# Kernel optimization log

Measured on AMD Instinct MI355X. Metric: run time of the kernel, lower is better.

The kernel has to match this reference:

```python
import jax, jax.numpy as jnp
from jax import lax
import numpy as np

H = 64
NS = 20000
NR = 2000
T = 24
ALPHA = 0.5


def _p(key, *shape):
    return jax.random.normal(key, shape, dtype=jnp.float32) * 0.05


def setup_inputs() -> dict:
    key = jax.random.key(0)
    ks = jax.random.split(key, 40)
    inp = {
        "x_store": jax.random.normal(ks[0], (NS, T), dtype=jnp.float32),
        "x_region": jax.random.normal(ks[1], (NR, T), dtype=jnp.float32),
        "edge_ss": jax.random.randint(ks[2], (2, 640000), 0, NS),
        "edge_rs_src": jax.random.randint(ks[3], (160000,), 0, NR),
        "edge_rs_dst": jax.random.randint(ks[4], (160000,), 0, NS),
        "edge_sr_src": jax.random.randint(ks[5], (160000,), 0, NS),
        "edge_sr_dst": jax.random.randint(ks[6], (160000,), 0, NR),
        # LSTM pretransform params (torch gate order i,f,g,o)
        "Wih_s": _p(ks[7], 4 * H, 1), "Whh_s": _p(ks[8], 4 * H, H),
        "bih_s": _p(ks[9], 4 * H), "bhh_s": _p(ks[10], 4 * H),
        "Wih_r": _p(ks[11], 4 * H, 1), "Whh_r": _p(ks[12], 4 * H, H),
        "bih_r": _p(ks[13], 4 * H), "bhh_r": _p(ks[14], 4 * H),
        # DirSageConv (store-store)
        "W_s2d": _p(ks[15], H, H), "b_s2d": _p(ks[16], H),
        "W_d2s": _p(ks[17], H, H), "b_d2s": _p(ks[18], H),
        "W_self": _p(ks[19], H, H), "b_self": _p(ks[20], H),
        # SAGEConv region->store (lin_l w/ bias, lin_r no bias)
        "Wl_rs": _p(ks[21], H, H), "bl_rs": _p(ks[22], H), "Wr_rs": _p(ks[23], H, H),
        # SAGEConv store->region
        "Wl_sr": _p(ks[24], H, H), "bl_sr": _p(ks[25], H), "Wr_sr": _p(ks[26], H, H),
        # final linear
        "Wf": _p(ks[27], H, H), "bf": _p(ks[28], H),
    }
    return inp


def lstm_last(x, Wih, Whh, bih, bhh):
    # x: [N, T] scalar sequences (input_size=1). Returns last hidden state [N, H].
    N = x.shape[0]
    w_in = Wih[:, 0]  # [4H]
    b = bih + bhh

    def step(carry, xt):
        h, c = carry
        gates = xt[:, None] * w_in[None, :] + h @ Whh.T + b  # [N, 4H]
        i, f, g, o = jnp.split(gates, 4, axis=1)
        c = jax.nn.sigmoid(f) * c + jax.nn.sigmoid(i) * jnp.tanh(g)
        h = jax.nn.sigmoid(o) * jnp.tanh(c)
        return (h, c), None

    z = jnp.zeros((N, Whh.shape[1]), x.dtype)
    (h, _), _ = lax.scan(step, (z, z), x.T)
    return h


def mean_aggr(feats, dst_idx, num_dst):
    # mean of gathered edge messages per destination node (0 for isolated nodes)
    s = jax.ops.segment_sum(feats, dst_idx, num_segments=num_dst)
    cnt = jax.ops.segment_sum(jnp.ones(dst_idx.shape, feats.dtype), dst_idx, num_segments=num_dst)
    return s / jnp.maximum(cnt, 1.0)[:, None]


def reference(x_store, x_region, edge_ss, edge_rs_src, edge_rs_dst,
              edge_sr_src, edge_sr_dst,
              Wih_s, Whh_s, bih_s, bhh_s, Wih_r, Whh_r, bih_r, bhh_r,
              W_s2d, b_s2d, W_d2s, b_d2s, W_self, b_self,
              Wl_rs, bl_rs, Wr_rs, Wl_sr, bl_sr, Wr_sr, Wf, bf):
    # per-node-type LSTM pretransform -> [N, H]
    hs = lstm_last(x_store, Wih_s, Whh_s, bih_s, bhh_s)
    hr = lstm_last(x_region, Wih_r, Whh_r, bih_r, bhh_r)

    # DirSageConv on (store, link, store)
    src, dst = edge_ss[0], edge_ss[1]
    a_fwd = mean_aggr(hs[src], dst, NS) @ W_s2d.T + b_s2d   # src -> dst
    a_rev = mean_aggr(hs[dst], src, NS) @ W_d2s.T + b_d2s   # dst -> src
    dir_out = hs @ W_self.T + b_self + (1.0 - ALPHA) * a_fwd + ALPHA * a_rev

    # SAGEConv (region, influences, store)
    rs_out = mean_aggr(hr[edge_rs_src], edge_rs_dst, NS) @ Wl_rs.T + bl_rs + hs @ Wr_rs.T

    # SAGEConv (store, rev_influences, region)
    sr_out = mean_aggr(hs[edge_sr_src], edge_sr_dst, NR) @ Wl_sr.T + bl_sr + hr @ Wr_sr.T

    # HeteroConv aggr='mean' over edge types per dst node type
    store_h = (dir_out + rs_out) * 0.5
    region_h = sr_out

    # residual + relu
    store_h = jax.nn.relu(store_h + hs)
    region_h = jax.nn.relu(region_h + hr)  # computed as in torch, unused by output

    return store_h @ Wf.T + bf
```

## Files before the change

kernel.cpp:

```cpp
#include <hip/hip_runtime.h>
#include <hip/hip_bf16.h>

#define TT 24
#define NSTORE 20000
#define NREGION 2000
#define NE_SS 640000
#define NE_RS 160000
#define BN 32
#define CAPF 80
#define CAPS 32
#define POISON ((int)0xAAAAAAAAu)

typedef __attribute__((ext_vector_type(8))) short bf16x8;
typedef __attribute__((ext_vector_type(4))) float f32x4;
typedef __attribute__((ext_vector_type(4))) int int4v;

__device__ __forceinline__ float rcpf(float x) { return __builtin_amdgcn_rcpf(x); }
__device__ __forceinline__ float sigm(float x) { return rcpf(1.0f + __expf(-x)); }
__device__ __forceinline__ float tanh_(float x) { return fmaf(-2.0f, rcpf(1.0f + __expf(2.0f * x)), 1.0f); }

__device__ __forceinline__ short f2bs(float x) {
    __hip_bfloat16 h = __float2bfloat16(x);
    return *reinterpret_cast<short*>(&h);
}
__device__ __forceinline__ bf16x8 pack8(float4 a, float4 b) {
    bf16x8 r;
    r[0] = f2bs(a.x); r[1] = f2bs(a.y); r[2] = f2bs(a.z); r[3] = f2bs(a.w);
    r[4] = f2bs(b.x); r[5] = f2bs(b.y); r[6] = f2bs(b.z); r[7] = f2bs(b.w);
    return r;
}
__device__ __forceinline__ unsigned packbf2(float lo, float hi) {
    return ((unsigned)(unsigned short)f2bs(hi) << 16) | (unsigned)(unsigned short)f2bs(lo);
}
__device__ __forceinline__ float bf_lo(unsigned u) { return __uint_as_float(u << 16); }
__device__ __forceinline__ float bf_hi(unsigned u) { return __uint_as_float(u & 0xffff0000u); }

__device__ __forceinline__ f32x4 mfma16(bf16x8 a, bf16x8 b, f32x4 c) {
    return __builtin_amdgcn_mfma_f32_16x16x32_bf16(a, b, c, 0, 0, 0);
}

__global__ __launch_bounds__(256)
void lstm_fill(const float* __restrict__ xs, const float* __restrict__ WihS,
               const float* __restrict__ WhhS, const float* __restrict__ bihS,
               const float* __restrict__ bhhS,
               const float* __restrict__ xr, const float* __restrict__ WihR,
               const float* __restrict__ WhhR, const float* __restrict__ bihR,
               const float* __restrict__ bhhR,
               unsigned* __restrict__ hsOut, unsigned* __restrict__ hrOut,
               const int* __restrict__ ss_src, const int* __restrict__ ss_dst,
               const int* __restrict__ rs_src, const int* __restrict__ rs_dst,
               int* __restrict__ curF, int* __restrict__ curR, int* __restrict__ curS,
               int* __restrict__ eidF, int* __restrict__ eidR, int* __restrict__ eidS,
               int nBlocksStore, int nBlocksLstm)
{
    const int tid = threadIdx.x;

    if ((int)blockIdx.x >= nBlocksLstm) {
        const int u = ((int)blockIdx.x - nBlocksLstm) * 256 + tid;
        if (u < NE_SS / 4) {
            const int4v s4 = __builtin_nontemporal_load(&((const int4v*)ss_src)[u]);
            const int4v d4 = __builtin_nontemporal_load(&((const int4v*)ss_dst)[u]);
            int pf0 = atomicAdd(&curF[d4[0]], 1) - POISON;
            int pf1 = atomicAdd(&curF[d4[1]], 1) - POISON;
            int pf2 = atomicAdd(&curF[d4[2]], 1) - POISON;
            int pf3 = atomicAdd(&curF[d4[3]], 1) - POISON;
            int pr0 = atomicAdd(&curR[s4[0]], 1) - POISON;
            int pr1 = atomicAdd(&curR[s4[1]], 1) - POISON;
            int pr2 = atomicAdd(&curR[s4[2]], 1) - POISON;
            int pr3 = atomicAdd(&curR[s4[3]], 1) - POISON;
            if (pf0 < CAPF) eidF[d4[0] * CAPF + pf0] = s4[0];
            if (pf1 < CAPF) eidF[d4[1] * CAPF + pf1] = s4[1];
            if (pf2 < CAPF) eidF[d4[2] * CAPF + pf2] = s4[2];
            if (pf3 < CAPF) eidF[d4[3] * CAPF + pf3] = s4[3];
            if (pr0 < CAPF) eidR[s4[0] * CAPF + pr0] = d4[0];
            if (pr1 < CAPF) eidR[s4[1] * CAPF + pr1] = d4[1];
            if (pr2 < CAPF) eidR[s4[2] * CAPF + pr2] = d4[2];
            if (pr3 < CAPF) eidR[s4[3] * CAPF + pr3] = d4[3];
        } else if (u < (NE_SS + NE_RS) / 4) {
            const int v = u - NE_SS / 4;
            const int4v s4 = __builtin_nontemporal_load(&((const int4v*)rs_src)[v]);
            const int4v d4 = __builtin_nontemporal_load(&((const int4v*)rs_dst)[v]);
            int p0 = atomicAdd(&curS[d4[0]], 1) - POISON;
            int p1 = atomicAdd(&curS[d4[1]], 1) - POISON;
            int p2 = atomicAdd(&curS[d4[2]], 1) - POISON;
            int p3 = atomicAdd(&curS[d4[3]], 1) - POISON;
            if (p0 < CAPS) eidS[d4[0] * CAPS + p0] = s4[0];
            if (p1 < CAPS) eidS[d4[1] * CAPS + p1] = s4[1];
            if (p2 < CAPS) eidS[d4[2] * CAPS + p2] = s4[2];
            if (p3 < CAPS) eidS[d4[3] * CAPS + p3] = s4[3];
        }
        return;
    }

    __shared__ unsigned hbU[2][32][36];
    __shared__ float xbuf[BN][25];

    const float *x, *Wih, *Whh, *bih, *bhh;
    unsigned* hout; int N, node0;
    if ((int)blockIdx.x < nBlocksStore) {
        x = xs; Wih = WihS; Whh = WhhS; bih = bihS; bhh = bhhS;
        hout = hsOut; N = NSTORE; node0 = blockIdx.x * BN;
    } else {
        x = xr; Wih = WihR; Whh = WhhR; bih = bihR; bhh = bhhR;
        hout = hrOut; N = NREGION; node0 = ((int)blockIdx.x - nBlocksStore) * BN;
    }

    const int w = tid >> 6, lane = tid & 63;
    const int l15 = lane & 15, q = lane >> 4;

    for (int i = tid; i < BN * TT; i += 256) {
        int n = i / TT, t = i - n * TT;
        int gn = node0 + n;
        xbuf[n][t] = (gn < N) ? x[gn * TT + t] : 0.0f;
    }

    bf16x8 Bf[4][2];
    #pragma unroll
    for (int g = 0; g < 4; ++g)
        #pragma unroll
        for (int kt = 0; kt < 2; ++kt) {
            const float* wrow = Whh + (g * 64 + (w << 4) + l15) * 64 + q * 8 + kt * 32;
            float4 v0 = *(const float4*)wrow;
            float4 v1 = *(const float4*)(wrow + 4);
            Bf[g][kt] = pack8(v0, v1);
        }

    float win[4], bsum[4];
    #pragma unroll
    for (int g = 0; g < 4; ++g) {
        int gi = g * 64 + (w << 4) + l15;
        win[g]  = Wih[gi];
        bsum[g] = bih[gi] + bhh[gi];
    }

    __syncthreads();

    float cc[2][4], hv[2][4];
    #pragma unroll
    for (int m = 0; m < 2; ++m)
        #pragma unroll
        for (int r = 0; r < 4; ++r) cc[m][r] = 0.0f;

    for (int t = 0; t < TT; ++t) {
        const int cur = t & 1, prev = cur ^ 1;

        bf16x8 Af[2][2];
        if (t > 0) {
            #pragma unroll
            for (int m = 0; m < 2; ++m)
                #pragma unroll
                for (int kt = 0; kt < 2; ++kt)
                    Af[m][kt] = *(const bf16x8*)&hbU[prev][l15 + 16 * m][(q << 2) + (kt << 4)];
        }

        f32x4 acc[4][2];
        float xv[2][4];
        #pragma unroll
        for (int m = 0; m < 2; ++m)
            #pragma unroll
            for (int r = 0; r < 4; ++r) xv[m][r] = xbuf[16 * m + q * 4 + r][t];
        #pragma unroll
        for (int g = 0; g < 4; ++g)
            #pragma unroll
            for (int m = 0; m < 2; ++m)
                #pragma unroll
                for (int r = 0; r < 4; ++r)
                    acc[g][m][r] = fmaf(xv[m][r], win[g], bsum[g]);

        if (t > 0) {
            #pragma unroll
            for (int g = 0; g < 4; ++g)
                #pragma unroll
                for (int m = 0; m < 2; ++m) {
                    acc[g][m] = mfma16(Af[m][0], Bf[g][0], acc[g][m]);
                    acc[g][m] = mfma16(Af[m][1], Bf[g][1], acc[g][m]);
                }
        }

        #pragma unroll
        for (int m = 0; m < 2; ++m)
            #pragma unroll
            for (int r = 0; r < 4; ++r) {
                float ig = sigm(acc[0][m][r]);
                float fg = sigm(acc[1][m][r]);
                float gg = tanh_(acc[2][m][r]);
                float og = sigm(acc[3][m][r]);
                float cn = fmaf(fg, cc[m][r], ig * gg);
                cc[m][r] = cn;
                hv[m][r] = og * tanh_(cn);
            }

        #pragma unroll
        for (int m = 0; m < 2; ++m)
            #pragma unroll
            for (int r = 0; r < 4; ++r) {
                float other = __shfl_xor(hv[m][r], 1);
                if ((l15 & 1) == 0)
                    hbU[cur][16 * m + 4 * q + r][(w << 3) + (l15 >> 1)] = packbf2(hv[m][r], other);
            }
        __syncthreads();
    }

    for (int i = tid; i < 32 * 32; i += 256) {
        int n = i >> 5, kp = i & 31;
        int gn = node0 + n;
        if (gn < N) hout[gn * 32 + kp] = hbU[1][n][kp];
    }
}

__global__ __launch_bounds__(256)
void gather_means(const unsigned* __restrict__ hsU, const unsigned* __restrict__ hrU,
                  const int* __restrict__ curF, const int* __restrict__ curR,
                  const int* __restrict__ curS,
                  const int* __restrict__ eidF, const int* __restrict__ eidR,
                  const int* __restrict__ eidS,
                  unsigned* __restrict__ xcatU)
{
    const int id = blockIdx.x * 4 + (threadIdx.x >> 6);
    const int lane = threadIdx.x & 63;
    const int sec = id / NSTORE;
    const int n   = id - sec * NSTORE;
    const int o8 = lane >> 3, l7 = lane & 7;

    unsigned* row = xcatU + (size_t)n * 128;

    if (sec == 0 && lane < 32) row[lane] = hsU[n * 32 + lane];

    const unsigned* feat = (sec == 2) ? hrU : hsU;
    const int* seg; int cnt, cap;
    if (sec == 0)      { seg = eidF + n * CAPF; cnt = curF[n] - POISON; cap = CAPF; }
    else if (sec == 1) { seg = eidR + n * CAPF; cnt = curR[n] - POISON; cap = CAPF; }
    else               { seg = eidS + n * CAPS; cnt = curS[n] - POISON; cap = CAPS; }
    int e = cnt < cap ? cnt : cap;

    float a[8];
    #pragma unroll
    for (int k = 0; k < 8; ++k) a[k] = 0.0f;

    for (int i = 0; i < e; i += 16) {
        int i0 = i + o8;
        if (i0 < e) {
            uint4 u = *(const uint4*)&feat[seg[i0] * 32 + 4 * l7];
            a[0] += bf_lo(u.x); a[1] += bf_hi(u.x);
            a[2] += bf_lo(u.y); a[3] += bf_hi(u.y);
            a[4] += bf_lo(u.z); a[5] += bf_hi(u.z);
            a[6] += bf_lo(u.w); a[7] += bf_hi(u.w);
        }
        int i1 = i + 8 + o8;
        if (i1 < e) {
            uint4 u = *(const uint4*)&feat[seg[i1] * 32 + 4 * l7];
            a[0] += bf_lo(u.x); a[1] += bf_hi(u.x);
            a[2] += bf_lo(u.y); a[3] += bf_hi(u.y);
            a[4] += bf_lo(u.z); a[5] += bf_hi(u.z);
            a[6] += bf_lo(u.w); a[7] += bf_hi(u.w);
        }
    }
    #pragma unroll
    for (int k = 0; k < 8; ++k) {
        a[k] += __shfl_xor(a[k], 8);
        a[k] += __shfl_xor(a[k], 16);
        a[k] += __shfl_xor(a[k], 32);
    }
    float c = rcpf(fmaxf((float)cnt, 1.0f));
    if (lane < 8) {
        uint4 o;
        o.x = packbf2(a[0] * c, a[1] * c);
        o.y = packbf2(a[2] * c, a[3] * c);
        o.z = packbf2(a[4] * c, a[5] * c);
        o.w = packbf2(a[6] * c, a[7] * c);
        *(uint4*)&row[(sec + 1) * 32 + 4 * l7] = o;
    }
}

__global__ __launch_bounds__(256, 3)
void combine_mm(const unsigned* __restrict__ xcatU,
                const float* __restrict__ Ws2d, const float* __restrict__ bs2d,
                const float* __restrict__ Wd2s, const float* __restrict__ bd2s,
                const float* __restrict__ Wself, const float* __restrict__ bself,
                const float* __restrict__ Wlrs, const float* __restrict__ blrs,
                const float* __restrict__ Wrrs,
                const float* __restrict__ Wfm, const float* __restrict__ bfv,
                float* __restrict__ out)
{
    __shared__ float Xs[64][36];
    __shared__ float Ps[64][64];
    __shared__ float Us[64][36];
    __shared__ float Wfs[64][68];
    __shared__ float biasc[64];

    const int tid = threadIdx.x;
    const int node0 = blockIdx.x * 32;

    for (int i = tid; i < 4096; i += 256) {
        int jp = i >> 6, j = i & 63;
        Wfs[j][jp] = Wfm[i];
    }
    if (tid < 64)
        biasc[tid] = bself[tid] + 0.5f * bs2d[tid] + 0.5f * bd2s[tid] + blrs[tid];

    const int jg = tid & 15, ng = tid >> 4;
    const int j0 = jg * 4, n0 = ng * 2;

    float acc[2][4];
    #pragma unroll
    for (int dn = 0; dn < 2; ++dn)
        #pragma unroll
        for (int dj = 0; dj < 4; ++dj) acc[dn][dj] = 0.0f;

    const int sj = tid >> 2, skb = tid & 3;

    for (int ci = 0; ci < 4; ++ci) {
        const int c = (ci + 1) & 3;
        __syncthreads();

        {
            int n = tid >> 3;
            int gn = node0 + n; if (gn > NSTORE - 1) gn = NSTORE - 1;
            const unsigned* src = xcatU + (size_t)gn * 128 + c * 32 + (tid & 7) * 4;
            uint4 u = *(const uint4*)src;
            unsigned uu[4] = {u.x, u.y, u.z, u.w};
            int k0 = (tid & 7) * 8;
            #pragma unroll
            for (int e = 0; e < 4; ++e) {
                Xs[k0 + 2 * e][n]     = bf_lo(uu[e]);
                Xs[k0 + 2 * e + 1][n] = bf_hi(uu[e]);
            }
        }
        {
            const float* W1; float scale;
            if (c == 0)      { W1 = Wself; scale = 1.0f; }
            else if (c == 1) { W1 = Ws2d;  scale = 0.5f; }
            else if (c == 2) { W1 = Wd2s;  scale = 0.5f; }
            else             { W1 = Wlrs;  scale = 1.0f; }
            #pragma unroll
            for (int qq = 0; qq < 4; ++qq) {
                int k0 = skb * 16 + qq * 4;
                float4 v = *(const float4*)(W1 + sj * 64 + k0);
                if (c == 0) {
                    float4 v2 = *(const float4*)(Wrrs + sj * 64 + k0);
                    v.x += v2.x; v.y += v2.y; v.z += v2.z; v.w += v2.w;
                } else {
                    v.x *= scale; v.y *= scale; v.z *= scale; v.w *= scale;
                }
                Ps[k0][sj] = v.x; Ps[k0 + 1][sj] = v.y;
                Ps[k0 + 2][sj] = v.z; Ps[k0 + 3][sj] = v.w;
            }
        }
        __syncthreads();

        #pragma unroll 4
        for (int k = 0; k < 64; ++k) {
            float4 wv = *(const float4*)&Ps[k][j0];
            float x0 = Xs[k][n0], x1 = Xs[k][n0 + 1];
            float w4[4] = {wv.x, wv.y, wv.z, wv.w};
            #pragma unroll
            for (int dj = 0; dj < 4; ++dj) {
                acc[0][dj] = fmaf(x0, w4[dj], acc[0][dj]);
                acc[1][dj] = fmaf(x1, w4[dj], acc[1][dj]);
            }
        }
    }

    #pragma unroll
    for (int dn = 0; dn < 2; ++dn)
        #pragma unroll
        for (int dj = 0; dj < 4; ++dj) {
            float h = Xs[j0 + dj][n0 + dn];
            float u = fmaxf(fmaf(0.5f, acc[dn][dj] + biasc[j0 + dj], h), 0.0f);
            Us[j0 + dj][n0 + dn] = u;
        }
    __syncthreads();

    float o[2][4];
    #pragma unroll
    for (int dn = 0; dn < 2; ++dn)
        #pragma unroll
        for (int dj = 0; dj < 4; ++dj) o[dn][dj] = 0.0f;

    #pragma unroll 4
    for (int k = 0; k < 64; ++k) {
        float4 wv = *(const float4*)&Wfs[k][j0];
        float u0 = Us[k][n0], u1 = Us[k][n0 + 1];
        float w4[4] = {wv.x, wv.y, wv.z, wv.w};
        #pragma unroll
        for (int dj = 0; dj < 4; ++dj) {
            o[0][dj] = fmaf(u0, w4[dj], o[0][dj]);
            o[1][dj] = fmaf(u1, w4[dj], o[1][dj]);
        }
    }

    float4 bfe = *(const float4*)(bfv + j0);
    #pragma unroll
    for (int dn = 0; dn < 2; ++dn) {
        int gn = node0 + n0 + dn;
        if (gn < NSTORE) {
            float4 v = make_float4(o[dn][0] + bfe.x, o[dn][1] + bfe.y,
                                   o[dn][2] + bfe.z, o[dn][3] + bfe.w);
            *(float4*)&out[gn * 64 + j0] = v;
        }
    }
}

extern "C" void kernel_launch(void* const* d_in, const int* in_sizes, int n_in,
                              void* d_out, int out_size, void* d_ws, size_t ws_size,
                              hipStream_t stream)
{
    const float* xs     = (const float*)d_in[0];
    const float* xr     = (const float*)d_in[1];
    const int*   e_ss   = (const int*)d_in[2];
    const int*   rs_src = (const int*)d_in[3];
    const int*   rs_dst = (const int*)d_in[4];
    const float* WihS = (const float*)d_in[7];
    const float* WhhS = (const float*)d_in[8];
    const float* bihS = (const float*)d_in[9];
    const float* bhhS = (const float*)d_in[10];
    const float* WihR = (const float*)d_in[11];
    const float* WhhR = (const float*)d_in[12];
    const float* bihR = (const float*)d_in[13];
    const float* bhhR = (const float*)d_in[14];
    const float* Ws2d = (const float*)d_in[15];
    const float* bs2d = (const float*)d_in[16];
    const float* Wd2s = (const float*)d_in[17];
    const float* bd2s = (const float*)d_in[18];
    const float* Wself = (const float*)d_in[19];
    const float* bself = (const float*)d_in[20];
    const float* Wlrs = (const float*)d_in[21];
    const float* blrs = (const float*)d_in[22];
    const float* Wrrs = (const float*)d_in[23];
    const float* Wfm = (const float*)d_in[27];
    const float* bfv = (const float*)d_in[28];

    const int* ss_src = e_ss;
    const int* ss_dst = e_ss + NE_SS;

    unsigned* hsU   = (unsigned*)d_ws;
    unsigned* hrU   = hsU + 640000;
    unsigned* xcatU = hrU + 64000;
    int*      ib    = (int*)(xcatU + 2560000);
    int* curF = ib;
    int* curR = ib + 20000;
    int* curS = ib + 40000;
    int* eidF = ib + 60000;
    int* eidR = eidF + NSTORE * CAPF;
    int* eidS = eidR + NSTORE * CAPF;

    const int storeBlocks  = (NSTORE + BN - 1) / BN;
    const int regionBlocks = (NREGION + BN - 1) / BN;
    const int lstmBlocks   = storeBlocks + regionBlocks;
    const int fillBlocks   = ((NE_SS + NE_RS) / 4 + 255) / 256;

    lstm_fill<<<lstmBlocks + fillBlocks, 256, 0, stream>>>(
        xs, WihS, WhhS, bihS, bhhS, xr, WihR, WhhR, bihR, bhhR,
        hsU, hrU, ss_src, ss_dst, rs_src, rs_dst,
        curF, curR, curS, eidF, eidR, eidS,
        storeBlocks, lstmBlocks);

    gather_means<<<3 * NSTORE / 4, 256, 0, stream>>>(hsU, hrU,
                                                     curF, curR, curS,
                                                     eidF, eidR, eidS, xcatU);

    combine_mm<<<(NSTORE + 31) / 32, 256, 0, stream>>>(xcatU,
                                                       Ws2d, bs2d, Wd2s, bd2s,
                                                       Wself, bself, Wlrs, blrs, Wrrs,
                                                       Wfm, bfv, (float*)d_out);
}
```

Measured before the change: 261.5 us.

## Fuse neighbor mean gathering into combine matmul kernel via shared memory

Merges the gather_means and combine_mm kernels into one 512-thread kernel. Each block gathers the three neighbor means for its 32 store nodes straight into shared memory in fp32, then runs the weight combine and final linear layer. This removes the xcatU global round trip, the bf16 rounding of the means, and one kernel launch. In exchange there are fewer blocks (625), each block must gather before it can compute with no overlap, and shared memory use per block grows, which may lower occupancy.

```diff
diff --git a/kernel.cpp b/kernel.cpp
--- a/kernel.cpp
+++ b/kernel.cpp
@@ -208,124 +208,106 @@
     }
 }
 
-__global__ __launch_bounds__(256)
-void gather_means(const unsigned* __restrict__ hsU, const unsigned* __restrict__ hrU,
-                  const int* __restrict__ curF, const int* __restrict__ curR,
-                  const int* __restrict__ curS,
-                  const int* __restrict__ eidF, const int* __restrict__ eidR,
-                  const int* __restrict__ eidS,
-                  unsigned* __restrict__ xcatU)
+__global__ __launch_bounds__(512)
+void gather_combine(const unsigned* __restrict__ hsU, const unsigned* __restrict__ hrU,
+                    const int* __restrict__ curF, const int* __restrict__ curR,
+                    const int* __restrict__ curS,
+                    const int* __restrict__ eidF, const int* __restrict__ eidR,
+                    const int* __restrict__ eidS,
+                    const float* __restrict__ Ws2d, const float* __restrict__ bs2d,
+                    const float* __restrict__ Wd2s, const float* __restrict__ bd2s,
+                    const float* __restrict__ Wself, const float* __restrict__ bself,
+                    const float* __restrict__ Wlrs, const float* __restrict__ blrs,
+                    const float* __restrict__ Wrrs,
+                    const float* __restrict__ Wfm, const float* __restrict__ bfv,
+                    float* __restrict__ out)
 {
-    const int id = blockIdx.x * 4 + (threadIdx.x >> 6);
-    const int lane = threadIdx.x & 63;
-    const int sec = id / NSTORE;
-    const int n   = id - sec * NSTORE;
-    const int o8 = lane >> 3, l7 = lane & 7;
-
-    unsigned* row = xcatU + (size_t)n * 128;
-
-    if (sec == 0 && lane < 32) row[lane] = hsU[n * 32 + lane];
-
-    const unsigned* feat = (sec == 2) ? hrU : hsU;
-    const int* seg; int cnt, cap;
-    if (sec == 0)      { seg = eidF + n * CAPF; cnt = curF[n] - POISON; cap = CAPF; }
-    else if (sec == 1) { seg = eidR + n * CAPF; cnt = curR[n] - POISON; cap = CAPF; }
-    else               { seg = eidS + n * CAPS; cnt = curS[n] - POISON; cap = CAPS; }
-    int e = cnt < cap ? cnt : cap;
-
-    float a[8];
-    #pragma unroll
-    for (int k = 0; k < 8; ++k) a[k] = 0.0f;
-
-    for (int i = 0; i < e; i += 16) {
-        int i0 = i + o8;
-        if (i0 < e) {
-            uint4 u = *(const uint4*)&feat[seg[i0] * 32 + 4 * l7];
-            a[0] += bf_lo(u.x); a[1] += bf_hi(u.x);
-            a[2] += bf_lo(u.y); a[3] += bf_hi(u.y);
-            a[4] += bf_lo(u.z); a[5] += bf_hi(u.z);
-            a[6] += bf_lo(u.w); a[7] += bf_hi(u.w);
-        }
-        int i1 = i + 8 + o8;
-        if (i1 < e) {
-            uint4 u = *(const uint4*)&feat[seg[i1] * 32 + 4 * l7];
-            a[0] += bf_lo(u.x); a[1] += bf_hi(u.x);
-            a[2] += bf_lo(u.y); a[3] += bf_hi(u.y);
-            a[4] += bf_lo(u.z); a[5] += bf_hi(u.z);
-            a[6] += bf_lo(u.w); a[7] += bf_hi(u.w);
-        }
-    }
-    #pragma unroll
-    for (int k = 0; k < 8; ++k) {
-        a[k] += __shfl_xor(a[k], 8);
-        a[k] += __shfl_xor(a[k], 16);
-        a[k] += __shfl_xor(a[k], 32);
-    }
-    float c = rcpf(fmaxf((float)cnt, 1.0f));
-    if (lane < 8) {
-        uint4 o;
-        o.x = packbf2(a[0] * c, a[1] * c);
-        o.y = packbf2(a[2] * c, a[3] * c);
-        o.z = packbf2(a[4] * c, a[5] * c);
-        o.w = packbf2(a[6] * c, a[7] * c);
-        *(uint4*)&row[(sec + 1) * 32 + 4 * l7] = o;
-    }
-}
-
-__global__ __launch_bounds__(256, 3)
-void combine_mm(const unsigned* __restrict__ xcatU,
-                const float* __restrict__ Ws2d, const float* __restrict__ bs2d,
-                const float* __restrict__ Wd2s, const float* __restrict__ bd2s,
-                const float* __restrict__ Wself, const float* __restrict__ bself,
-                const float* __restrict__ Wlrs, const float* __restrict__ blrs,
-                const float* __restrict__ Wrrs,
-                const float* __restrict__ Wfm, const float* __restrict__ bfv,
-                float* __restrict__ out)
-{
-    __shared__ float Xs[64][36];
+    __shared__ float Xsec[3][64][33];
+    __shared__ float Xh[64][33];
     __shared__ float Ps[64][64];
-    __shared__ float Us[64][36];
+    __shared__ float Us[64][33];
     __shared__ float Wfs[64][68];
     __shared__ float biasc[64];
 
     const int tid = threadIdx.x;
     const int node0 = blockIdx.x * 32;
 
-    for (int i = tid; i < 4096; i += 256) {
+    for (int i = tid; i < 4096; i += 512) {
         int jp = i >> 6, j = i & 63;
         Wfs[j][jp] = Wfm[i];
     }
     if (tid < 64)
         biasc[tid] = bself[tid] + 0.5f * bs2d[tid] + 0.5f * bd2s[tid] + blrs[tid];
 
-    const int jg = tid & 15, ng = tid >> 4;
-    const int j0 = jg * 4, n0 = ng * 2;
-
-    float acc[2][4];
-    #pragma unroll
-    for (int dn = 0; dn < 2; ++dn)
-        #pragma unroll
-        for (int dj = 0; dj < 4; ++dj) acc[dn][dj] = 0.0f;
-
-    const int sj = tid >> 2, skb = tid & 3;
-
-    for (int ci = 0; ci < 4; ++ci) {
-        const int c = (ci + 1) & 3;
+    for (int i = tid; i < 32 * 32; i += 512) {
+        int n = i >> 5, kp = i & 31;
+        unsigned u = hsU[(node0 + n) * 32 + kp];
+        Xh[2 * kp][n]     = bf_lo(u);
+        Xh[2 * kp + 1][n] = bf_hi(u);
+    }
+
+    const int w8 = tid >> 6, lane = tid & 63;
+    const int o8 = lane >> 3, l7 = lane & 7;
+
+    #pragma unroll 1
+    for (int j = 0; j < 12; ++j) {
+        const int task = w8 * 12 + j;
+        const int sec = task >> 5;
+        const int tn  = task & 31;
+        const int n   = node0 + tn;
+
+        const unsigned* feat = (sec == 2) ? hrU : hsU;
+        const int* seg; int cnt, cap;
+        if (sec == 0)      { seg = eidF + n * CAPF; cnt = curF[n] - POISON; cap = CAPF; }
+        else if (sec == 1) { seg = eidR + n * CAPF; cnt = curR[n] - POISON; cap = CAPF; }
+        else               { seg = eidS + n * CAPS; cnt = curS[n] - POISON; cap = CAPS; }
+        int e = cnt < cap ? cnt : cap;
+
+        float a[8];
+        #pragma unroll
+        for (int k = 0; k < 8; ++k) a[k] = 0.0f;
+
+        for (int i = 0; i < e; i += 16) {
+            int i0 = i + o8;
+            if (i0 < e) {
+                uint4 u = *(const uint4*)&feat[seg[i0] * 32 + 4 * l7];
+                a[0] += bf_lo(u.x); a[1] += bf_hi(u.x);
+                a[2] += bf_lo(u.y); a[3] += bf_hi(u.y);
+                a[4] += bf_lo(u.z); a[5] += bf_hi(u.z);
+                a[6] += bf_lo(u.w); a[7] += bf_hi(u.w);
+            }
+            int i1 = i + 8 + o8;
+            if (i1 < e) {
+                uint4 u = *(const uint4*)&feat[seg[i1] * 32 + 4 * l7];
+                a[0] += bf_lo(u.x); a[1] += bf_hi(u.x);
+                a[2] += bf_lo(u.y); a[3] += bf_hi(u.y);
+                a[4] += bf_lo(u.z); a[5] += bf_hi(u.z);
+                a[6] += bf_lo(u.w); a[7] += bf_hi(u.w);
+            }
+        }
+        #pragma unroll
+        for (int k = 0; k < 8; ++k) {
+            a[k] += __shfl_xor(a[k], 8);
+            a[k] += __shfl_xor(a[k], 16);
+            a[k] += __shfl_xor(a[k], 32);
+        }
+        float c = rcpf(fmaxf((float)cnt, 1.0f));
+        if (lane < 8) {
+            #pragma unroll
+            for (int k = 0; k < 8; ++k)
+                Xsec[sec][8 * lane + k][tn] = a[k] * c;
+        }
+    }
+    __syncthreads();
+
+    const int jg = tid & 15, j0 = jg * 4;
+    const int nn = tid >> 4;
+    const int sj = tid >> 3, sk8 = tid & 7;
+
+    float acc[4] = {0.0f, 0.0f, 0.0f, 0.0f};
+
+    for (int c = 0; c < 4; ++c) {
         __syncthreads();
-
-        {
-            int n = tid >> 3;
-            int gn = node0 + n; if (gn > NSTORE - 1) gn = NSTORE - 1;
-            const unsigned* src = xcatU + (size_t)gn * 128 + c * 32 + (tid & 7) * 4;
-            uint4 u = *(const uint4*)src;
-            unsigned uu[4] = {u.x, u.y, u.z, u.w};
-            int k0 = (tid & 7) * 8;
-            #pragma unroll
-            for (int e = 0; e < 4; ++e) {
-                Xs[k0 + 2 * e][n]     = bf_lo(uu[e]);
-                Xs[k0 + 2 * e + 1][n] = bf_hi(uu[e]);
-            }
-        }
         {
             const float* W1; float scale;
             if (c == 0)      { W1 = Wself; scale = 1.0f; }
@@ -333,8 +315,8 @@
             else if (c == 2) { W1 = Wd2s;  scale = 0.5f; }
             else             { W1 = Wlrs;  scale = 1.0f; }
             #pragma unroll
-            for (int qq = 0; qq < 4; ++qq) {
-                int k0 = skb * 16 + qq * 4;
+            for (int qq = 0; qq < 2; ++qq) {
+                int k0 = sk8 * 8 + qq * 4;
                 float4 v = *(const float4*)(W1 + sj * 64 + k0);
                 if (c == 0) {
                     float4 v2 = *(const float4*)(Wrrs + sj * 64 + k0);
@@ -348,57 +330,41 @@
         }
         __syncthreads();
 
+        const float (*Xc)[33] = (c == 0) ? Xh : Xsec[c - 1];
         #pragma unroll 4
         for (int k = 0; k < 64; ++k) {
             float4 wv = *(const float4*)&Ps[k][j0];
-            float x0 = Xs[k][n0], x1 = Xs[k][n0 + 1];
-            float w4[4] = {wv.x, wv.y, wv.z, wv.w};
-            #pragma unroll
-            for (int dj = 0; dj < 4; ++dj) {
-                acc[0][dj] = fmaf(x0, w4[dj], acc[0][dj]);
-                acc[1][dj] = fmaf(x1, w4[dj], acc[1][dj]);
-            }
+            float xv = Xc[k][nn];
+            acc[0] = fmaf(xv, wv.x, acc[0]);
+            acc[1] = fmaf(xv, wv.y, acc[1]);
+            acc[2] = fmaf(xv, wv.z, acc[2]);
+            acc[3] = fmaf(xv, wv.w, acc[3]);
         }
     }
 
     #pragma unroll
-    for (int dn = 0; dn < 2; ++dn)
-        #pragma unroll
-        for (int dj = 0; dj < 4; ++dj) {
-            float h = Xs[j0 + dj][n0 + dn];
-            float u = fmaxf(fmaf(0.5f, acc[dn][dj] + biasc[j0 + dj], h), 0.0f);
-            Us[j0 + dj][n0 + dn] = u;
-        }
+    for (int dj = 0; dj < 4; ++dj) {
+        float h = Xh[j0 + dj][nn];
+        Us[j0 + dj][nn] = fmaxf(fmaf(0.5f, acc[dj] + biasc[j0 + dj], h), 0.0f);
+    }
     __syncthreads();
 
-    float o[2][4];
-    #pragma unroll
-    for (int dn = 0; dn < 2; ++dn)
-        #pragma unroll
-        for (int dj = 0; dj < 4; ++dj) o[dn][dj] = 0.0f;
-
+    float o[4] = {0.0f, 0.0f, 0.0f, 0.0f};
     #pragma unroll 4
     for (int k = 0; k < 64; ++k) {
         float4 wv = *(const float4*)&Wfs[k][j0];
-        float u0 = Us[k][n0], u1 = Us[k][n0 + 1];
-        float w4[4] = {wv.x, wv.y, wv.z, wv.w};
-        #pragma unroll
-        for (int dj = 0; dj < 4; ++dj) {
-            o[0][dj] = fmaf(u0, w4[dj], o[0][dj]);
-            o[1][dj] = fmaf(u1, w4[dj], o[1][dj]);
-        }
+        float uv = Us[k][nn];
+        o[0] = fmaf(uv, wv.x, o[0]);
+        o[1] = fmaf(uv, wv.y, o[1]);
+        o[2] = fmaf(uv, wv.z, o[2]);
+        o[3] = fmaf(uv, wv.w, o[3]);
     }
 
     float4 bfe = *(const float4*)(bfv + j0);
-    #pragma unroll
-    for (int dn = 0; dn < 2; ++dn) {
-        int gn = node0 + n0 + dn;
-        if (gn < NSTORE) {
-            float4 v = make_float4(o[dn][0] + bfe.x, o[dn][1] + bfe.y,
-                                   o[dn][2] + bfe.z, o[dn][3] + bfe.w);
-            *(float4*)&out[gn * 64 + j0] = v;
-        }
-    }
+    const int gn = node0 + nn;
+    float4 v = make_float4(o[0] + bfe.x, o[1] + bfe.y,
+                           o[2] + bfe.z, o[3] + bfe.w);
+    *(float4*)&out[gn * 64 + j0] = v;
 }
 
 extern "C" void kernel_launch(void* const* d_in, const int* in_sizes, int n_in,
@@ -455,12 +421,10 @@
         curF, curR, curS, eidF, eidR, eidS,
         storeBlocks, lstmBlocks);
 
-    gather_means<<<3 * NSTORE / 4, 256, 0, stream>>>(hsU, hrU,
-                                                     curF, curR, curS,
-                                                     eidF, eidR, eidS, xcatU);
-
-    combine_mm<<<(NSTORE + 31) / 32, 256, 0, stream>>>(xcatU,
-                                                       Ws2d, bs2d, Wd2s, bd2s,
-                                                       Wself, bself, Wlrs, blrs, Wrrs,
-                                                       Wfm, bfv, (float*)d_out);
-}
+    gather_combine<<<NSTORE / 32, 512, 0, stream>>>(hsU, hrU,
+                                                    curF, curR, curS,
+                                                    eidF, eidR, eidS,
+                                                    Ws2d, bs2d, Wd2s, bd2s,
+                                                    Wself, bself, Wlrs, blrs, Wrrs,
+                                                    Wfm, bfv, (float*)d_out);
+}
```

Measured after the change: 294.2 us. +12.5%, slower.
